# Kernel tuning notes

Hardware: AMD Instinct MI355X
Metric: run time of the kernel (lower is better)

## Reference

```python
import jax, jax.numpy as jnp
from jax import lax
import numpy as np

L, D_LOCAL, BOND, BATCH = 64, 2, 64, 4096
STDDEV = 0.01  # default_kernel_init = normal(stddev=0.01)


def setup_inputs() -> dict:
    key = jax.random.key(0)
    k1, k2 = jax.random.split(key)
    x = jax.random.randint(k1, (BATCH, L), 0, D_LOCAL, dtype=jnp.int32)
    tensors_param = STDDEV * jax.random.normal(k2, (L, D_LOCAL, BOND, BOND), dtype=jnp.float32)
    return {"x": x, "tensors_param": tensors_param}


def reference(x, tensors_param):
    # tensors = param + identity (as in setup())
    P, d, D, _ = tensors_param.shape
    tensors = tensors_param + jnp.eye(D, dtype=tensors_param.dtype)  # [P, d, D, D]
    Lx = x.shape[-1]
    # tile unit cell across the chain (symperiod == L here, so tile factor is 1)
    all_tensors = jnp.tile(tensors, (Lx // P, 1, 1, 1))  # [L, d, D, D]
    B = x.shape[0]
    edge0 = jnp.broadcast_to(jnp.eye(D, dtype=tensors.dtype), (B, D, D))

    def step(edge, pair):
        t, qn = pair                      # t: [d, D, D], qn: [B]
        A = t[qn]                         # gather local matrices -> [B, D, D]
        return jnp.einsum('bij,bjk->bik', edge, A), None

    edge, _ = lax.scan(step, edge0, (all_tensors, x.T))  # scan over L sites
    psi = jnp.trace(edge, axis1=-2, axis2=-1)            # [B]
    return jnp.log(psi.astype(jnp.complex64))
```

## Files before the change

kernel.cpp:

```cpp
#include <hip/hip_runtime.h>


typedef __attribute__((ext_vector_type(8))) __bf16 bf16x8;
typedef __attribute__((ext_vector_type(4))) float f32x4;
typedef __attribute__((ext_vector_type(4))) int   int4v;

#define MFMA16(a, b, c) __builtin_amdgcn_mfma_f32_16x16x32_bf16((a), (b), (c), 0, 0, 0)

union frag_u { int4v i; bf16x8 v; };

__device__ __forceinline__ unsigned short f2bf(float f) {
  union { float f; unsigned u; } v; v.f = f;
  unsigned r = v.u + 0x7fffu + ((v.u >> 16) & 1u);
  return (unsigned short)(r >> 16);
}

__global__ __launch_bounds__(256) void prep_kernel(const float* __restrict__ p,
                                                   unsigned short* __restrict__ Tn,
                                                   unsigned short* __restrict__ Tt) {
  int t = blockIdx.x * 256 + threadIdx.x;
  int j  = t & 63;
  int i  = (t >> 6) & 63;
  int pq = t >> 12;
  float v = p[t] + ((i == j) ? 1.0f : 0.0f);
  unsigned short h = f2bf(v);
  Tn[t] = h;
  Tt[(((size_t)pq) << 12) + (size_t)j * 64 + i] = h;
}

__global__ __launch_bounds__(64) void pairprod_kernel(const unsigned short* __restrict__ inN,
                                                      const unsigned short* __restrict__ inT,
                                                      unsigned short* __restrict__ outN,
                                                      unsigned short* __restrict__ outT,
                                                      int inCombos) {
  const int w  = blockIdx.x;
  const int oc = inCombos * inCombos;
  const int s  = w / oc, c = w % oc;
  const int cl = c / inCombos, cr = c % inCombos;
  const unsigned short* X = inN + (((size_t)(2 * s * inCombos + cl)) << 12);
  const unsigned short* Y = inT + (((size_t)((2 * s + 1) * inCombos + cr)) << 12);
  const int l = threadIdx.x & 63, lm = l & 15, lq = l >> 4;

  f32x4 acc[4][4] = {};
#pragma unroll
  for (int ks = 0; ks < 2; ++ks) {
    bf16x8 A[4], B[4];
#pragma unroll
    for (int t = 0; t < 4; ++t) {
      A[t] = *reinterpret_cast<const bf16x8*>(X + (16 * t + lm) * 64 + 32 * ks + 8 * lq);
      B[t] = *reinterpret_cast<const bf16x8*>(Y + (16 * t + lm) * 64 + 32 * ks + 8 * lq);
    }
#pragma unroll
    for (int ti = 0; ti < 4; ++ti)
#pragma unroll
      for (int tj = 0; tj < 4; ++tj)
        acc[ti][tj] = MFMA16(A[ti], B[tj], acc[ti][tj]);
  }

  unsigned short* OT = outT + (((size_t)w) << 12);
#pragma unroll
  for (int ti = 0; ti < 4; ++ti)
#pragma unroll
    for (int tj = 0; tj < 4; ++tj) {
      int n = 16 * tj + lm, m0 = 16 * ti + 4 * lq;
      ushort4 pk;
      pk.x = f2bf(acc[ti][tj][0]);
      pk.y = f2bf(acc[ti][tj][1]);
      pk.z = f2bf(acc[ti][tj][2]);
      pk.w = f2bf(acc[ti][tj][3]);
      *reinterpret_cast<ushort4*>(OT + (size_t)n * 64 + m0) = pk;
    }

  if (outN != nullptr) {
    unsigned short* ON = outN + (((size_t)w) << 12);
#pragma unroll
    for (int ti = 0; ti < 4; ++ti)
#pragma unroll
      for (int tj = 0; tj < 4; ++tj) {
        int row0 = 16 * ti + 4 * lq, col = 16 * tj + lm;
#pragma unroll
        for (int r = 0; r < 4; ++r)
          ON[(size_t)(row0 + r) * 64 + col] = f2bf(acc[ti][tj][r]);
      }
  }
}

__global__ __launch_bounds__(256) void chain_wave_kernel(const int* __restrict__ x,
                                                         const unsigned short* __restrict__ P8n,
                                                         const unsigned short* __restrict__ P8t,
                                                         float* __restrict__ out) {
  const int tid = threadIdx.x;
  const int l   = tid & 63;
  const int b   = blockIdx.x * 4 + (tid >> 6);
  const int c   = l & 15;
  const int p   = l >> 4;

  unsigned long long mask = __ballot((x[b * 64 + l] & 1) != 0);
  int idx[8];
#pragma unroll
  for (int s = 0; s < 8; ++s) {
    unsigned byte = (unsigned)((mask >> (8 * s)) & 0xFFull);
    idx[s] = (int)(__builtin_bitreverse32(byte) >> 24);
  }

  const int srcA = (l & 15) | ((l & 16) << 1);
  const int srcB = srcA | 16;
  const bool hi5 = (l & 32) != 0;

  frag_u B[2][4];
  {
    const unsigned short* base = P8t + (((size_t)(7 * 256 + idx[7])) << 12);
#pragma unroll
    for (int ks = 0; ks < 2; ++ks)
#pragma unroll
      for (int nj = 0; nj < 4; ++nj)
        B[ks][nj].i = *reinterpret_cast<const int4v*>(base + (c + 16 * nj) * 64 + 32 * ks + 8 * p);
  }

#pragma unroll
  for (int s = 6; s >= 1; --s) {
    const unsigned short* abase = P8n + (((size_t)(s * 256 + idx[s])) << 12);
    frag_u A[4][2];
#pragma unroll
    for (int mi = 0; mi < 4; ++mi)
#pragma unroll
      for (int ks = 0; ks < 2; ++ks)
        A[mi][ks].i = *reinterpret_cast<const int4v*>(abase + (c + 16 * mi) * 64 + 32 * ks + 8 * p);

    int pk[4][4][2];
#pragma unroll
    for (int mi = 0; mi < 4; ++mi)
#pragma unroll
      for (int nj = 0; nj < 4; ++nj) {
        f32x4 d = {0.f, 0.f, 0.f, 0.f};
        d = MFMA16(A[mi][0].v, B[0][nj].v, d);
        d = MFMA16(A[mi][1].v, B[1][nj].v, d);
        asm("v_cvt_pk_bf16_f32 %0, %1, %2" : "=v"(pk[mi][nj][0]) : "v"(d[0]), "v"(d[1]));
        asm("v_cvt_pk_bf16_f32 %0, %1, %2" : "=v"(pk[mi][nj][1]) : "v"(d[2]), "v"(d[3]));
      }

#pragma unroll
    for (int ks = 0; ks < 2; ++ks)
#pragma unroll
      for (int nj = 0; nj < 4; ++nj) {
        int lo0 = pk[2 * ks][nj][0],     lo1 = pk[2 * ks][nj][1];
        int hi0 = pk[2 * ks + 1][nj][0], hi1 = pk[2 * ks + 1][nj][1];
        int a0 = __shfl(lo0, srcA, 64), b0 = __shfl(hi0, srcA, 64);
        int a1 = __shfl(lo1, srcA, 64), b1 = __shfl(hi1, srcA, 64);
        int a2 = __shfl(lo0, srcB, 64), b2 = __shfl(hi0, srcB, 64);
        int a3 = __shfl(lo1, srcB, 64), b3 = __shfl(hi1, srcB, 64);
        int4v nb = { hi5 ? b0 : a0, hi5 ? b1 : a1, hi5 ? b2 : a2, hi5 ? b3 : a3 };
        B[ks][nj].i = nb;
      }
  }

  float psum = 0.f;
  {
    const unsigned short* abase = P8n + (((size_t)idx[0]) << 12);
#pragma unroll
    for (int t = 0; t < 4; ++t) {
      frag_u A0, A1;
      A0.i = *reinterpret_cast<const int4v*>(abase + (c + 16 * t) * 64 + 0  + 8 * p);
      A1.i = *reinterpret_cast<const int4v*>(abase + (c + 16 * t) * 64 + 32 + 8 * p);
      f32x4 d = {0.f, 0.f, 0.f, 0.f};
      d = MFMA16(A0.v, B[0][t].v, d);
      d = MFMA16(A1.v, B[1][t].v, d);
      if (p == (c >> 2)) {
#pragma unroll
        for (int r = 0; r < 4; ++r) psum += (r == (c & 3)) ? d[r] : 0.f;
      }
    }
  }
#pragma unroll
  for (int o = 32; o > 0; o >>= 1) psum += __shfl_down(psum, o, 64);
  if (l == 0) out[b] = logf(fabsf(psum));
}

extern "C" void kernel_launch(void* const* d_in, const int* in_sizes, int n_in,
                              void* d_out, int out_size, void* d_ws, size_t ws_size,
                              hipStream_t stream) {
  const int*   x     = (const int*)d_in[0];
  const float* param = (const float*)d_in[1];
  float* out = (float*)d_out;

  char* ws = (char*)d_ws;
  unsigned short* Tn  = (unsigned short*)(ws + (0ull  << 20));
  unsigned short* Tt  = (unsigned short*)(ws + (1ull  << 20));
  unsigned short* P2n = (unsigned short*)(ws + (2ull  << 20));
  unsigned short* P2t = (unsigned short*)(ws + (3ull  << 20));
  unsigned short* P4n = (unsigned short*)(ws + (4ull  << 20));
  unsigned short* P4t = (unsigned short*)(ws + (6ull  << 20));
  unsigned short* P8n = (unsigned short*)(ws + (8ull  << 20));
  unsigned short* P8t = (unsigned short*)(ws + (24ull << 20));

  prep_kernel<<<2048, 256, 0, stream>>>(param, Tn, Tt);
  pairprod_kernel<<<128,  64, 0, stream>>>(Tn,  Tt,  P2n, P2t, 2);
  pairprod_kernel<<<256,  64, 0, stream>>>(P2n, P2t, P4n, P4t, 4);
  pairprod_kernel<<<2048, 64, 0, stream>>>(P4n, P4t, P8n, P8t, 16);
  chain_wave_kernel<<<1024, 256, 0, stream>>>(x, P8n, P8t, out);
}
```

Measured before the change: 67.47 us.

## Build 8-site product table directly in one kernel instead of three pair levels

Replaces the three-level pairwise product tree (P2, P4, P8) with a single kernel. Each wave computes one 8-site combination directly from the base site matrices by chaining 7 matmuls in registers, reusing the chain kernel's shuffle-based fragment transpose. This removes two kernel launches and the intermediate P2/P4 global round trips. In exchange it does more MFMA work per entry (7 products rather than 1 per level) and applies bf16 rounding at every step of the chain rather than only at each tree level.

```diff
diff --git a/kernel.cpp b/kernel.cpp
--- a/kernel.cpp
+++ b/kernel.cpp
@@ -28,59 +28,99 @@
   Tt[(((size_t)pq) << 12) + (size_t)j * 64 + i] = h;
 }
 
-__global__ __launch_bounds__(64) void pairprod_kernel(const unsigned short* __restrict__ inN,
-                                                      const unsigned short* __restrict__ inT,
-                                                      unsigned short* __restrict__ outN,
-                                                      unsigned short* __restrict__ outT,
-                                                      int inCombos) {
-  const int w  = blockIdx.x;
-  const int oc = inCombos * inCombos;
-  const int s  = w / oc, c = w % oc;
-  const int cl = c / inCombos, cr = c % inCombos;
-  const unsigned short* X = inN + (((size_t)(2 * s * inCombos + cl)) << 12);
-  const unsigned short* Y = inT + (((size_t)((2 * s + 1) * inCombos + cr)) << 12);
-  const int l = threadIdx.x & 63, lm = l & 15, lq = l >> 4;
-
-  f32x4 acc[4][4] = {};
-#pragma unroll
-  for (int ks = 0; ks < 2; ++ks) {
-    bf16x8 A[4], B[4];
-#pragma unroll
-    for (int t = 0; t < 4; ++t) {
-      A[t] = *reinterpret_cast<const bf16x8*>(X + (16 * t + lm) * 64 + 32 * ks + 8 * lq);
-      B[t] = *reinterpret_cast<const bf16x8*>(Y + (16 * t + lm) * 64 + 32 * ks + 8 * lq);
-    }
-#pragma unroll
-    for (int ti = 0; ti < 4; ++ti)
-#pragma unroll
-      for (int tj = 0; tj < 4; ++tj)
-        acc[ti][tj] = MFMA16(A[ti], B[tj], acc[ti][tj]);
-  }
-
-  unsigned short* OT = outT + (((size_t)w) << 12);
-#pragma unroll
-  for (int ti = 0; ti < 4; ++ti)
-#pragma unroll
-    for (int tj = 0; tj < 4; ++tj) {
-      int n = 16 * tj + lm, m0 = 16 * ti + 4 * lq;
-      ushort4 pk;
-      pk.x = f2bf(acc[ti][tj][0]);
-      pk.y = f2bf(acc[ti][tj][1]);
-      pk.z = f2bf(acc[ti][tj][2]);
-      pk.w = f2bf(acc[ti][tj][3]);
-      *reinterpret_cast<ushort4*>(OT + (size_t)n * 64 + m0) = pk;
-    }
-
-  if (outN != nullptr) {
-    unsigned short* ON = outN + (((size_t)w) << 12);
-#pragma unroll
-    for (int ti = 0; ti < 4; ++ti)
-#pragma unroll
-      for (int tj = 0; tj < 4; ++tj) {
-        int row0 = 16 * ti + 4 * lq, col = 16 * tj + lm;
-#pragma unroll
-        for (int r = 0; r < 4; ++r)
-          ON[(size_t)(row0 + r) * 64 + col] = f2bf(acc[ti][tj][r]);
+__global__ __launch_bounds__(256) void build_p8_kernel(const unsigned short* __restrict__ Tn,
+                                                       const unsigned short* __restrict__ Tt,
+                                                       unsigned short* __restrict__ P8n,
+                                                       unsigned short* __restrict__ P8t) {
+  const int tid = threadIdx.x;
+  const int l   = tid & 63;
+  const int w   = blockIdx.x * 4 + (tid >> 6);
+  const int s   = w >> 8, cmb = w & 255;
+  const int c   = l & 15, p = l >> 4;
+
+  const int srcA = (l & 15) | ((l & 16) << 1);
+  const int srcB = srcA | 16;
+  const bool hi5 = (l & 32) != 0;
+
+  frag_u B[2][4];
+  {
+    int m7 = (8 * s + 7) * 2 + (cmb & 1);
+    const unsigned short* base = Tt + ((size_t)m7 << 12);
+#pragma unroll
+    for (int ks = 0; ks < 2; ++ks)
+#pragma unroll
+      for (int nj = 0; nj < 4; ++nj)
+        B[ks][nj].i = *reinterpret_cast<const int4v*>(base + (c + 16 * nj) * 64 + 32 * ks + 8 * p);
+  }
+
+#pragma unroll
+  for (int j = 6; j >= 1; --j) {
+    int m = (8 * s + j) * 2 + ((cmb >> (7 - j)) & 1);
+    const unsigned short* abase = Tn + ((size_t)m << 12);
+    frag_u A[4][2];
+#pragma unroll
+    for (int mi = 0; mi < 4; ++mi)
+#pragma unroll
+      for (int ks = 0; ks < 2; ++ks)
+        A[mi][ks].i = *reinterpret_cast<const int4v*>(abase + (c + 16 * mi) * 64 + 32 * ks + 8 * p);
+
+    int pk[4][4][2];
+#pragma unroll
+    for (int mi = 0; mi < 4; ++mi)
+#pragma unroll
+      for (int nj = 0; nj < 4; ++nj) {
+        f32x4 d = {0.f, 0.f, 0.f, 0.f};
+        d = MFMA16(A[mi][0].v, B[0][nj].v, d);
+        d = MFMA16(A[mi][1].v, B[1][nj].v, d);
+        asm("v_cvt_pk_bf16_f32 %0, %1, %2" : "=v"(pk[mi][nj][0]) : "v"(d[0]), "v"(d[1]));
+        asm("v_cvt_pk_bf16_f32 %0, %1, %2" : "=v"(pk[mi][nj][1]) : "v"(d[2]), "v"(d[3]));
+      }
+#pragma unroll
+    for (int ks = 0; ks < 2; ++ks)
+#pragma unroll
+      for (int nj = 0; nj < 4; ++nj) {
+        int lo0 = pk[2 * ks][nj][0],     lo1 = pk[2 * ks][nj][1];
+        int hi0 = pk[2 * ks + 1][nj][0], hi1 = pk[2 * ks + 1][nj][1];
+        int a0 = __shfl(lo0, srcA, 64), b0 = __shfl(hi0, srcA, 64);
+        int a1 = __shfl(lo1, srcA, 64), b1 = __shfl(hi1, srcA, 64);
+        int a2 = __shfl(lo0, srcB, 64), b2 = __shfl(hi0, srcB, 64);
+        int a3 = __shfl(lo1, srcB, 64), b3 = __shfl(hi1, srcB, 64);
+        int4v nb = { hi5 ? b0 : a0, hi5 ? b1 : a1, hi5 ? b2 : a2, hi5 ? b3 : a3 };
+        B[ks][nj].i = nb;
+      }
+  }
+
+  {
+    int m0 = (8 * s) * 2 + ((cmb >> 7) & 1);
+    const unsigned short* abase = Tn + ((size_t)m0 << 12);
+    frag_u A[4][2];
+#pragma unroll
+    for (int mi = 0; mi < 4; ++mi)
+#pragma unroll
+      for (int ks = 0; ks < 2; ++ks)
+        A[mi][ks].i = *reinterpret_cast<const int4v*>(abase + (c + 16 * mi) * 64 + 32 * ks + 8 * p);
+
+    unsigned short* ON = P8n + (((size_t)w) << 12);
+    unsigned short* OT = P8t + (((size_t)w) << 12);
+#pragma unroll
+    for (int mi = 0; mi < 4; ++mi)
+#pragma unroll
+      for (int nj = 0; nj < 4; ++nj) {
+        f32x4 d = {0.f, 0.f, 0.f, 0.f};
+        d = MFMA16(A[mi][0].v, B[0][nj].v, d);
+        d = MFMA16(A[mi][1].v, B[1][nj].v, d);
+        if (s < 7) {
+          int row0 = 16 * mi + 4 * p, col = 16 * nj + c;
+#pragma unroll
+          for (int r = 0; r < 4; ++r)
+            ON[(size_t)(row0 + r) * 64 + col] = f2bf(d[r]);
+        } else {
+          int n = 16 * nj + c, m0r = 16 * mi + 4 * p;
+          ushort4 pkv;
+          pkv.x = f2bf(d[0]); pkv.y = f2bf(d[1]);
+          pkv.z = f2bf(d[2]); pkv.w = f2bf(d[3]);
+          *reinterpret_cast<ushort4*>(OT + (size_t)n * 64 + m0r) = pkv;
+        }
       }
   }
 }
@@ -138,7 +178,6 @@
         asm("v_cvt_pk_bf16_f32 %0, %1, %2" : "=v"(pk[mi][nj][0]) : "v"(d[0]), "v"(d[1]));
         asm("v_cvt_pk_bf16_f32 %0, %1, %2" : "=v"(pk[mi][nj][1]) : "v"(d[2]), "v"(d[3]));
       }
-
 #pragma unroll
     for (int ks = 0; ks < 2; ++ks)
 #pragma unroll
@@ -186,16 +225,10 @@
   char* ws = (char*)d_ws;
   unsigned short* Tn  = (unsigned short*)(ws + (0ull  << 20));
   unsigned short* Tt  = (unsigned short*)(ws + (1ull  << 20));
-  unsigned short* P2n = (unsigned short*)(ws + (2ull  << 20));
-  unsigned short* P2t = (unsigned short*)(ws + (3ull  << 20));
-  unsigned short* P4n = (unsigned short*)(ws + (4ull  << 20));
-  unsigned short* P4t = (unsigned short*)(ws + (6ull  << 20));
   unsigned short* P8n = (unsigned short*)(ws + (8ull  << 20));
   unsigned short* P8t = (unsigned short*)(ws + (24ull << 20));
 
   prep_kernel<<<2048, 256, 0, stream>>>(param, Tn, Tt);
-  pairprod_kernel<<<128,  64, 0, stream>>>(Tn,  Tt,  P2n, P2t, 2);
-  pairprod_kernel<<<256,  64, 0, stream>>>(P2n, P2t, P4n, P4t, 4);
-  pairprod_kernel<<<2048, 64, 0, stream>>>(P4n, P4t, P8n, P8t, 16);
+  build_p8_kernel<<<512, 256, 0, stream>>>(Tn, Tt, P8n, P8t);
   chain_wave_kernel<<<1024, 256, 0, stream>>>(x, P8n, P8t, out);
 }
```

Measured after the change: 66.13 us. 1.02x faster.
